# Performance work log

Measured on AMD Instinct MI355X. Metric: run time of the kernel, lower is better.

The kernel has to match this reference:

```python
import jax, jax.numpy as jnp
import numpy as np

D_MODEL = 1024
NUM_HEADS = 16
D_K = D_MODEL // NUM_HEADS


def setup_inputs() -> dict:
    key = jax.random.key(0)
    ks = jax.random.split(key, 9)
    s = 1.0 / np.sqrt(D_MODEL)
    x = jax.random.normal(ks[0], (4, 2048, D_MODEL), dtype=jnp.float32)
    Wq = jax.random.uniform(ks[1], (D_MODEL, D_MODEL), jnp.float32, -s, s)
    bq = jax.random.uniform(ks[2], (D_MODEL,), jnp.float32, -s, s)
    Wk = jax.random.uniform(ks[3], (D_MODEL, D_MODEL), jnp.float32, -s, s)
    bk = jax.random.uniform(ks[4], (D_MODEL,), jnp.float32, -s, s)
    Wv = jax.random.uniform(ks[5], (D_MODEL, D_MODEL), jnp.float32, -s, s)
    bv = jax.random.uniform(ks[6], (D_MODEL,), jnp.float32, -s, s)
    Wo = jax.random.uniform(ks[7], (D_MODEL, D_MODEL), jnp.float32, -s, s)
    bo = jax.random.uniform(ks[8], (D_MODEL,), jnp.float32, -s, s)
    return {"x": x, "Wq": Wq, "bq": bq, "Wk": Wk, "bk": bk,
            "Wv": Wv, "bv": bv, "Wo": Wo, "bo": bo}


def reference(x, Wq, bq, Wk, bk, Wv, bv, Wo, bo):
    B, T, C = x.shape
    H, Dk = NUM_HEADS, D_K
    # linear projections (torch Linear: x @ W.T + b; here W stored as [in,out])
    q = (x @ Wq + bq).reshape(B, T, H, Dk).transpose(0, 2, 1, 3)  # [B,H,T,Dk]
    k = (x @ Wk + bk).reshape(B, T, H, Dk).transpose(0, 2, 1, 3)
    v = (x @ Wv + bv).reshape(B, T, H, Dk).transpose(0, 2, 1, 3)
    scores = jnp.einsum("bhtd,bhsd->bhts", q, k) / jnp.sqrt(jnp.float32(Dk))
    attn = jax.nn.softmax(scores, axis=-1)  # [B,H,T,T]
    context = jnp.einsum("bhts,bhsd->bhtd", attn, v)
    context = context.transpose(0, 2, 1, 3).reshape(B, T, C)
    return context @ Wo + bo
```

## Files before the change

### kernel.cpp

```cpp
#include <hip/hip_runtime.h>
#include <hip/hip_bf16.h>
#include <stdint.h>

typedef short bf16x8 __attribute__((ext_vector_type(8)));
typedef short bf16x4 __attribute__((ext_vector_type(4)));
typedef float f32x4  __attribute__((ext_vector_type(4)));

#define MFMA16(a, b, c) __builtin_amdgcn_mfma_f32_16x16x32_bf16((a), (b), (c), 0, 0, 0)

#if __has_builtin(__builtin_amdgcn_mfma_f32_16x16x16bf16_1k)
  #define HAVE_K16 1
  #define MFMAK16(a, b, c) __builtin_amdgcn_mfma_f32_16x16x16bf16_1k((a), (b), (c), 0, 0, 0)
#elif __has_builtin(__builtin_amdgcn_mfma_f32_16x16x16_bf16)
  #define HAVE_K16 1
  #define MFMAK16(a, b, c) __builtin_amdgcn_mfma_f32_16x16x16_bf16((a), (b), (c), 0, 0, 0)
#else
  #define HAVE_K16 0
#endif

__device__ __forceinline__ unsigned short f2bf(float f) {
    union { float f; unsigned int u; } v; v.f = f;
    unsigned int u = v.u;
    u += 0x7fffu + ((u >> 16) & 1u);
    return (unsigned short)(u >> 16);
}

__device__ __forceinline__ unsigned int trunc_pk(float a, float b) {
    return (__float_as_uint(a) >> 16) | (__float_as_uint(b) & 0xffff0000u);
}

__device__ __forceinline__ float exp2f_fast(float x) {
#if __has_builtin(__builtin_amdgcn_exp2f)
    return __builtin_amdgcn_exp2f(x);
#else
    return exp2f(x);
#endif
}

__device__ __forceinline__ void g2lds16(const void* g, void* l) {
    __builtin_amdgcn_global_load_lds(
        (const __attribute__((address_space(1))) void*)g,
        (__attribute__((address_space(3))) void*)l, 16, 0, 0);
}


__global__ __launch_bounds__(256) void convert_x_kernel(
    const float4* __restrict__ src, ushort4* __restrict__ dst)
{
    int i = blockIdx.x * 256 + threadIdx.x;
    float4 v = src[i];
    ushort4 o;
    o.x = f2bf(v.x); o.y = f2bf(v.y); o.z = f2bf(v.z); o.w = f2bf(v.w);
    dst[i] = o;
}

__global__ __launch_bounds__(256) void transpose_w4_kernel(
    const float* __restrict__ W0, const float* __restrict__ W1,
    const float* __restrict__ W2, const float* __restrict__ W3,
    unsigned short* __restrict__ dst_base)
{
    __shared__ float tile[64][65];
    const int z = blockIdx.z;
    const float* src = (z == 0) ? W0 : (z == 1) ? W1 : (z == 2) ? W2 : W3;
    unsigned short* dst = dst_base + ((size_t)z << 20);
    const int k0 = blockIdx.x * 64, n0 = blockIdx.y * 64;
    const int tx = threadIdx.x & 63, ty = threadIdx.x >> 6;
    #pragma unroll
    for (int i = 0; i < 64; i += 4)
        tile[ty + i][tx] = src[(size_t)(k0 + ty + i) * 1024 + n0 + tx];
    __syncthreads();
    #pragma unroll
    for (int i = 0; i < 64; i += 4)
        dst[(size_t)(n0 + ty + i) * 1024 + k0 + tx] = f2bf(tile[tx][ty + i]);
}


#define QSCALE 0.18033688011112042f

template <int MODE>
__global__ __launch_bounds__(256, 2) void gemm_bt(
    const unsigned short* __restrict__ A, const unsigned short* __restrict__ Bt,
    const float* __restrict__ b0, const float* __restrict__ b1, const float* __restrict__ b2,
    unsigned short* __restrict__ Qb, unsigned short* __restrict__ Kb,
    unsigned short* __restrict__ Vt, float* __restrict__ out)
{
    __shared__ alignas(16) unsigned short As[128 * 32];
    __shared__ alignas(16) unsigned short Bs[128 * 32];

    const int t = threadIdx.x;
    const int m0 = blockIdx.y * 128, n0 = blockIdx.x * 128;
    const int lane = t & 63, w = t >> 6, quad = lane >> 4, c16 = lane & 15;
    const int moff = (w >> 1) * 64, noff = (w & 1) * 64;

    f32x4 acc[4][4];
    #pragma unroll
    for (int i = 0; i < 4; ++i)
        #pragma unroll
        for (int j = 0; j < 4; ++j)
            acc[i][j] = (f32x4){0.f, 0.f, 0.f, 0.f};

    const unsigned short* Ag = A + (size_t)(m0 + (t >> 2)) * 1024 + (t & 3) * 8;
    const unsigned short* Bg = Bt + (size_t)(n0 + (t >> 2)) * 1024 + (t & 3) * 8;
    unsigned short* Asl = As + t * 8;
    unsigned short* Bsl = Bs + t * 8;

    for (int k0 = 0; k0 < 1024; k0 += 32) {
        g2lds16(Ag + k0,             Asl);
        g2lds16(Ag + 64 * 1024 + k0, Asl + 2048);
        g2lds16(Bg + k0,             Bsl);
        g2lds16(Bg + 64 * 1024 + k0, Bsl + 2048);
        __syncthreads();

        bf16x8 af[4], bfr[4];
        #pragma unroll
        for (int ms = 0; ms < 4; ++ms)
            af[ms] = *(const bf16x8*)(As + (moff + ms * 16 + c16) * 32 + quad * 8);
        #pragma unroll
        for (int ns = 0; ns < 4; ++ns)
            bfr[ns] = *(const bf16x8*)(Bs + (noff + ns * 16 + c16) * 32 + quad * 8);
        #pragma unroll
        for (int ms = 0; ms < 4; ++ms)
            #pragma unroll
            for (int ns = 0; ns < 4; ++ns)
                acc[ms][ns] = MFMA16(af[ms], bfr[ns], acc[ms][ns]);
        __syncthreads();
    }

    #pragma unroll
    for (int ns = 0; ns < 4; ++ns) {
        const int n = n0 + noff + ns * 16 + c16;
        if (MODE == 0) {
            const int mat = n >> 10, nn = n & 1023;
            const int h = nn >> 6, d = nn & 63;
            const float bias = (mat == 0) ? b0[nn] : ((mat == 1) ? b1[nn] : b2[nn]);
            #pragma unroll
            for (int ms = 0; ms < 4; ++ms) {
                const int mbase = m0 + moff + ms * 16 + quad * 4;
                const int b = mbase >> 11, tbase = mbase & 2047;
                const int bh = b * 16 + h;
                if (mat == 2) {
                    ushort4 pk;
                    pk.x = f2bf(acc[ms][ns][0] + bias);
                    pk.y = f2bf(acc[ms][ns][1] + bias);
                    pk.z = f2bf(acc[ms][ns][2] + bias);
                    pk.w = f2bf(acc[ms][ns][3] + bias);
                    *(ushort4*)(Vt + ((size_t)bh * 64 + d) * 2048 + tbase) = pk;
                } else {
                    #pragma unroll
                    for (int r = 0; r < 4; ++r) {
                        float v = acc[ms][ns][r] + bias;
                        if (mat == 0) v *= QSCALE;
                        unsigned short* dst = (mat == 0) ? Qb : Kb;
                        dst[((size_t)bh * 2048 + tbase + r) * 64 + d] = f2bf(v);
                    }
                }
            }
        } else {
            const float bias = b0[n];
            #pragma unroll
            for (int ms = 0; ms < 4; ++ms) {
                #pragma unroll
                for (int r = 0; r < 4; ++r) {
                    const int m = m0 + moff + ms * 16 + quad * 4 + r;
                    out[(size_t)m * 1024 + n] = acc[ms][ns][r] + bias;
                }
            }
        }
    }
}


__global__ __launch_bounds__(128, 2) void attn_kernel(
    const unsigned short* __restrict__ Qb, const unsigned short* __restrict__ Kb,
    const unsigned short* __restrict__ Vt, unsigned short* __restrict__ ctx)
{
    __shared__ alignas(16) unsigned short Ks[64 * 64];
    __shared__ alignas(16) unsigned short Vs[64 * 64];

    const int t = threadIdx.x, w = t >> 6, lane = t & 63;
    const int quad = lane >> 4, c16 = lane & 15;
    const int L = blockIdx.y * 16 + blockIdx.x;
    const int bh = ((L & 7) << 3) + (L >> 7);
    const int qt = (L >> 3) & 15;
    const int qbase = qt * 128 + w * 64;

    bf16x8 qf[4][2];
    #pragma unroll
    for (int mt = 0; mt < 4; ++mt) {
        const unsigned short* Qp = Qb + ((size_t)bh * 2048 + qbase + mt * 16 + c16) * 64;
        qf[mt][0] = *(const bf16x8*)(Qp + quad * 8);
        qf[mt][1] = *(const bf16x8*)(Qp + 32 + quad * 8);
    }

    float l_r[4] = {0.f, 0.f, 0.f, 0.f};
    f32x4 O[4][4];
    #pragma unroll
    for (int mt = 0; mt < 4; ++mt)
        #pragma unroll
        for (int dc = 0; dc < 4; ++dc) O[mt][dc] = (f32x4){0.f, 0.f, 0.f, 0.f};

    const int sgrp = (t & 7) ^ ((t >> 3) & 7);
    const unsigned short* Kgl = Kb + (size_t)bh * 131072 + (size_t)(t >> 3) * 64 + sgrp * 8;
    const unsigned short* Vgl = Vt + (size_t)bh * 131072 + (size_t)(t >> 3) * 2048 + sgrp * 8;
    unsigned short* Ksl = Ks + t * 8;
    unsigned short* Vsl = Vs + t * 8;
    const f32x4 fzero = {0.f, 0.f, 0.f, 0.f};

    for (int s0 = 0; s0 < 2048; s0 += 64) {
        #pragma unroll
        for (int q = 0; q < 4; ++q) {
            g2lds16(Kgl + s0 * 64 + q * 1024,  Ksl + q * 1024);
            g2lds16(Vgl + s0 + q * 32768,      Vsl + q * 1024);
        }
        __syncthreads();

        #pragma unroll
        for (int ct = 0; ct < 4; ++ct) {
            const int key = ct * 16 + c16;
            const bf16x8 kf0 = *(const bf16x8*)(Ks + key * 64 + ((quad ^ (key & 7)) << 3));
            const bf16x8 kf1 = *(const bf16x8*)(Ks + key * 64 + (((4 + quad) ^ (key & 7)) << 3));

            uint2 vf[4];
            const int g = ct * 2 + (quad >> 1);
            #pragma unroll
            for (int dc = 0; dc < 4; ++dc) {
                const int d = dc * 16 + c16;
                vf[dc] = *(const uint2*)(Vs + d * 64 + ((g ^ (d & 7)) << 3) + (quad & 1) * 4);
            }

            #pragma unroll
            for (int mt = 0; mt < 4; ++mt) {
                f32x4 sa = MFMA16(kf0, qf[mt][0], fzero);
                sa = MFMA16(kf1, qf[mt][1], sa);
                const float p0 = exp2f_fast(sa[0]);
                const float p1 = exp2f_fast(sa[1]);
                const float p2 = exp2f_fast(sa[2]);
                const float p3 = exp2f_fast(sa[3]);
                l_r[mt] += (p0 + p1) + (p2 + p3);
#if HAVE_K16
                union { bf16x4 v; unsigned int d[2]; } af;
                af.d[0] = trunc_pk(p0, p1);
                af.d[1] = trunc_pk(p2, p3);
                #pragma unroll
                for (int dc = 0; dc < 4; ++dc) {
                    union { bf16x4 v; uint2 u; } bv;
                    bv.u = vf[dc];
                    O[mt][dc] = MFMAK16(af.v, bv.v, O[mt][dc]);
                }
#else
                union { bf16x8 v; unsigned int d[4]; } af;
                af.d[0] = trunc_pk(p0, p1);
                af.d[1] = trunc_pk(p2, p3);
                af.d[2] = 0u; af.d[3] = 0u;
                #pragma unroll
                for (int dc = 0; dc < 4; ++dc) {
                    union { bf16x8 v; uint2 u[2]; } bfv;
                    bfv.u[0] = vf[dc]; bfv.u[1] = vf[dc];
                    O[mt][dc] = MFMA16(af.v, bfv.v, O[mt][dc]);
                }
#endif
            }
        }
        __syncthreads();
    }

    #pragma unroll
    for (int mt = 0; mt < 4; ++mt) {
        l_r[mt] += __shfl_xor(l_r[mt], 16);
        l_r[mt] += __shfl_xor(l_r[mt], 32);
    }

    const int b = bh >> 4, h = bh & 15;
    #pragma unroll
    for (int mt = 0; mt < 4; ++mt) {
        float inv[4];
        #pragma unroll
        for (int r = 0; r < 4; ++r)
            inv[r] = 1.0f / __shfl(l_r[mt], quad * 4 + r);
        #pragma unroll
        for (int dc = 0; dc < 4; ++dc)
            #pragma unroll
            for (int r = 0; r < 4; ++r) {
                const int row = qbase + mt * 16 + quad * 4 + r;
                ctx[((size_t)(b * 2048 + row)) * 1024 + h * 64 + dc * 16 + c16] =
                    f2bf(O[mt][dc][r] * inv[r]);
            }
    }
}


extern "C" void kernel_launch(void* const* d_in, const int* in_sizes, int n_in,
                              void* d_out, int out_size, void* d_ws, size_t ws_size,
                              hipStream_t stream)
{
    const float* x  = (const float*)d_in[0];
    const float* Wq = (const float*)d_in[1];
    const float* bq = (const float*)d_in[2];
    const float* Wk = (const float*)d_in[3];
    const float* bk = (const float*)d_in[4];
    const float* Wv = (const float*)d_in[5];
    const float* bv = (const float*)d_in[6];
    const float* Wo = (const float*)d_in[7];
    const float* bo = (const float*)d_in[8];
    float* out = (float*)d_out;

    char* ws = (char*)d_ws;
    unsigned short* xb    = (unsigned short*)(ws);
    unsigned short* Wqkvt = (unsigned short*)(ws + (16u << 20));
    unsigned short* Vt    = (unsigned short*)(ws + (24u << 20));
    unsigned short* Wot   = Wqkvt + (3u << 20);
    unsigned short* Qb    = (unsigned short*)((char*)d_out);
    unsigned short* Kb    = (unsigned short*)((char*)d_out + (16u << 20));

    convert_x_kernel<<<8192, 256, 0, stream>>>((const float4*)x, (ushort4*)xb);
    transpose_w4_kernel<<<dim3(16, 16, 4), 256, 0, stream>>>(Wq, Wk, Wv, Wo, Wqkvt);

    gemm_bt<0><<<dim3(24, 64), 256, 0, stream>>>(xb, Wqkvt, bq, bk, bv, Qb, Kb, Vt, nullptr);
    attn_kernel<<<dim3(16, 64), 128, 0, stream>>>(Qb, Kb, Vt, xb );
    gemm_bt<1><<<dim3(8, 64), 256, 0, stream>>>(xb, Wot, bo, nullptr, nullptr,
                                                nullptr, nullptr, nullptr, out);
}
```

Baseline: 287.4 us.

## Double-buffer K/V tiles in attention kernel to overlap loads with MFMA

The attention kernel's K and V shared-memory tiles become ping-pong buffers. The next 64-key tile is issued with async global-to-LDS copies before the current tile is computed, and partial vmcnt waits replace full syncthreads. This is meant to hide global load latency behind the QK and PV MFMA work. The cost is double the LDS footprint (32KB per block), which could limit occupancy at 2 blocks per CU, plus hand-tuned waitcnt ordering that is easy to get wrong.

```diff
diff --git a/kernel.cpp b/kernel.cpp
--- a/kernel.cpp
+++ b/kernel.cpp
@@ -174,8 +174,8 @@
     const unsigned short* __restrict__ Qb, const unsigned short* __restrict__ Kb,
     const unsigned short* __restrict__ Vt, unsigned short* __restrict__ ctx)
 {
-    __shared__ alignas(16) unsigned short Ks[64 * 64];
-    __shared__ alignas(16) unsigned short Vs[64 * 64];
+    __shared__ alignas(16) unsigned short Ks[2][64 * 64];
+    __shared__ alignas(16) unsigned short Vs[2][64 * 64];
 
     const int t = threadIdx.x, w = t >> 6, lane = t & 63;
     const int quad = lane >> 4, c16 = lane & 15;
@@ -202,30 +202,49 @@
     const int sgrp = (t & 7) ^ ((t >> 3) & 7);
     const unsigned short* Kgl = Kb + (size_t)bh * 131072 + (size_t)(t >> 3) * 64 + sgrp * 8;
     const unsigned short* Vgl = Vt + (size_t)bh * 131072 + (size_t)(t >> 3) * 2048 + sgrp * 8;
-    unsigned short* Ksl = Ks + t * 8;
-    unsigned short* Vsl = Vs + t * 8;
+    const int tOff = t * 8;
     const f32x4 fzero = {0.f, 0.f, 0.f, 0.f};
 
-    for (int s0 = 0; s0 < 2048; s0 += 64) {
-        #pragma unroll
-        for (int q = 0; q < 4; ++q) {
-            g2lds16(Kgl + s0 * 64 + q * 1024,  Ksl + q * 1024);
-            g2lds16(Vgl + s0 + q * 32768,      Vsl + q * 1024);
+    #pragma unroll
+    for (int q = 0; q < 4; ++q) {
+        g2lds16(Kgl + q * 1024,  Ks[0] + tOff + q * 1024);
+        g2lds16(Vgl + q * 32768, Vs[0] + tOff + q * 1024);
+    }
+
+    for (int it = 0; it < 32; ++it) {
+        const int cur = it & 1;
+        const unsigned short* Kc = Ks[cur];
+        const unsigned short* Vc = Vs[cur];
+
+        if (it < 31) {
+            const int s0 = (it + 1) * 64;
+            unsigned short* Kn = Ks[cur ^ 1] + tOff;
+            unsigned short* Vn = Vs[cur ^ 1] + tOff;
+            #pragma unroll
+            for (int q = 0; q < 4; ++q) {
+                g2lds16(Kgl + (size_t)s0 * 64 + q * 1024, Kn + q * 1024);
+                g2lds16(Vgl + s0 + q * 32768,             Vn + q * 1024);
+            }
+            asm volatile("s_waitcnt vmcnt(8)" ::: "memory");
+        } else {
+            asm volatile("s_waitcnt vmcnt(0)" ::: "memory");
         }
-        __syncthreads();
+        __builtin_amdgcn_sched_barrier(0);
+        __builtin_amdgcn_s_barrier();
+        __builtin_amdgcn_sched_barrier(0);
 
         #pragma unroll
         for (int ct = 0; ct < 4; ++ct) {
             const int key = ct * 16 + c16;
-            const bf16x8 kf0 = *(const bf16x8*)(Ks + key * 64 + ((quad ^ (key & 7)) << 3));
-            const bf16x8 kf1 = *(const bf16x8*)(Ks + key * 64 + (((4 + quad) ^ (key & 7)) << 3));
+            const bf16x8 kf0 = *(const bf16x8*)(Kc + key * 64 + ((quad ^ (key & 7)) << 3));
+            const bf16x8 kf1 = *(const bf16x8*)(Kc + key * 64 + (((4 + quad) ^ (key & 7)) << 3));
 
             uint2 vf[4];
             const int g = ct * 2 + (quad >> 1);
             #pragma unroll
             for (int dc = 0; dc < 4; ++dc) {
                 const int d = dc * 16 + c16;
-                vf[dc] = *(const uint2*)(Vs + d * 64 + ((g ^ (d & 7)) << 3) + (quad & 1) * 4);
+                vf[dc] = *(const uint2*)(Vc + d * 64 + ((g ^ (d & 7)) << 3) + (quad & 1) * 4);
             }
 
             #pragma unroll
@@ -261,7 +280,13 @@
 #endif
             }
         }
-        __syncthreads();
+
+        if (it < 31) {
+            asm volatile("s_waitcnt lgkmcnt(0)" ::: "memory");
+            __builtin_amdgcn_sched_barrier(0);
+            __builtin_amdgcn_s_barrier();
+            __builtin_amdgcn_sched_barrier(0);
+        }
     }
 
     #pragma unroll
```

After: 284.1 us. About the same (-1.1%).
